# Optimization experiments

Measured on AMD Instinct MI355X. Metric: run time of the kernel, lower is better.

Reference implementation:

```python
import jax, jax.numpy as jnp
import numpy as np

ATOM_FDIM = 133
BOND_FDIM = 14
HIDDEN = 300
DEPTH = 3
FFN_HIDDEN = 300
NUM_ATOMS = 100000
NUM_EDGES = 400000
NUM_MOLS = 4096


def setup_inputs() -> dict:
    key = jax.random.key(0)
    ks = jax.random.split(key, 10)
    x = jax.random.normal(ks[0], (NUM_ATOMS, ATOM_FDIM), dtype=jnp.float32)
    edge_index = jax.random.randint(ks[1], (2, NUM_EDGES), 0, NUM_ATOMS, dtype=jnp.int32)
    edge_attr = jax.random.normal(ks[2], (NUM_EDGES, BOND_FDIM), dtype=jnp.float32)
    batch = jnp.sort(jax.random.randint(ks[3], (NUM_ATOMS,), 0, NUM_MOLS, dtype=jnp.int32))
    s = 0.05
    W_i = jax.random.normal(ks[4], (HIDDEN, ATOM_FDIM + BOND_FDIM), dtype=jnp.float32) * s
    W_h = jax.random.normal(ks[5], (HIDDEN, HIDDEN), dtype=jnp.float32) * s
    W_o_w = jax.random.normal(ks[6], (HIDDEN, ATOM_FDIM + HIDDEN), dtype=jnp.float32) * s
    W_o_b = jnp.zeros((HIDDEN,), dtype=jnp.float32)
    ffn1_w = jax.random.normal(ks[7], (FFN_HIDDEN, HIDDEN), dtype=jnp.float32) * s
    ffn1_b = jnp.zeros((FFN_HIDDEN,), dtype=jnp.float32)
    ffn2_w = jax.random.normal(ks[8], (1, FFN_HIDDEN), dtype=jnp.float32) * s
    ffn2_b = jnp.zeros((1,), dtype=jnp.float32)
    return {"x": x, "edge_index": edge_index, "edge_attr": edge_attr, "batch": batch,
            "W_i": W_i, "W_h": W_h, "W_o_w": W_o_w, "W_o_b": W_o_b,
            "ffn1_w": ffn1_w, "ffn1_b": ffn1_b, "ffn2_w": ffn2_w, "ffn2_b": ffn2_b}


def reference(x, edge_index, edge_attr, batch, W_i, W_h, W_o_w, W_o_b,
              ffn1_w, ffn1_b, ffn2_w, ffn2_b):
    num_atoms = x.shape[0]
    src, tgt = edge_index[0], edge_index[1]
    # initial edge messages: [E, hidden]
    init = jnp.concatenate([x[src], edge_attr], axis=-1)
    m = jax.nn.relu(init @ W_i.T)
    # dropout is identity at inference
    for _ in range(DEPTH - 1):
        nei = jax.ops.segment_sum(m, tgt, num_segments=num_atoms)  # [N, hidden]
        m = jax.nn.relu(m + nei[src] @ W_h.T)
    atom_msg = jax.ops.segment_sum(m, tgt, num_segments=num_atoms)
    atom_h = jax.nn.relu(jnp.concatenate([x, atom_msg], axis=-1) @ W_o_w.T + W_o_b)
    mol = jax.ops.segment_sum(atom_h, batch, num_segments=NUM_MOLS)  # [B, hidden]
    h = jax.nn.relu(mol @ ffn1_w.T + ffn1_b)
    out = h @ ffn2_w.T + ffn2_b  # [B, 1]
    return out
```

## Files before the change

kernel.cpp:

```cpp
#include <hip/hip_runtime.h>
#include <hip/hip_fp16.h>

#define HID   300
#define NEIP  320
#define PSTR  900
#define APB   4
#define SWK(r) (((r) >> 1) & 3)

typedef _Float16 f16;
typedef f16  f16x2 __attribute__((ext_vector_type(2)));
typedef f16  f16x4 __attribute__((ext_vector_type(4)));
typedef f16  f16x8 __attribute__((ext_vector_type(8)));
typedef float f32x4 __attribute__((ext_vector_type(4)));

__device__ __forceinline__ f16x2 u2h(unsigned u) {
    union { unsigned u; f16x2 h; } c; c.u = u; return c.h;
}
__device__ __forceinline__ unsigned pk16(float a, float b) {
    union { f16 h[2]; unsigned u; } c; c.h[0] = (f16)a; c.h[1] = (f16)b;
    return c.u;
}
__device__ __forceinline__ void glds16(const void* g, void* l) {
    __builtin_amdgcn_global_load_lds(
        (const __attribute__((address_space(1))) void*)g,
        (__attribute__((address_space(3))) void*)l, 16, 0, 0);
}

__global__ __launch_bounds__(256) void fill_f32(float* __restrict__ p, int n, float v)
{
    int i = blockIdx.x * blockDim.x + threadIdx.x;
    int stride = gridDim.x * blockDim.x;
    for (; i < n; i += stride) p[i] = v;
}

__global__ __launch_bounds__(256) void zero_i32(int* __restrict__ p, int n)
{
    int i = blockIdx.x * blockDim.x + threadIdx.x;
    int stride = gridDim.x * blockDim.x;
    for (; i < n; i += stride) p[i] = 0;
}

__global__ __launch_bounds__(256) void cvt_pad_f16(
    f16* __restrict__ dst, const float* __restrict__ src,
    int srcRows, int ldsrc, int kuse, int kpad, int dstRows)
{
    int i = blockIdx.x * 256 + threadIdx.x;
    const int total = dstRows * kpad;
    const int st = gridDim.x * 256;
    for (; i < total; i += st) {
        int r = i / kpad, k = i - r * kpad;
        float v = (r < srcRows && k < kuse) ? src[(size_t)r * ldsrc + k] : 0.f;
        const int t = k >> 5, kg = (k >> 3) & 3, w = k & 7;
        const int kd = (t << 5) | ((kg ^ SWK(r)) << 3) | w;
        dst[(size_t)r * kpad + kd] = (f16)v;
    }
}

__global__ __launch_bounds__(256) void hist_tgt(
    const int* __restrict__ tgt, int* __restrict__ deg, int E, int N)
{
    int e = blockIdx.x * 256 + threadIdx.x;
    const int st = gridDim.x * 256;
    for (; e < E; e += st) {
        int t = tgt[e];
        t = ((unsigned)t < (unsigned)N) ? t : 0;
        atomicAdd(&deg[t], 1);
    }
}

__global__ __launch_bounds__(1024) void scan_p1(
    const int* __restrict__ deg, int* __restrict__ bsum, int N)
{
    __shared__ int s[1024];
    const int t = threadIdx.x;
    const int i = blockIdx.x * 1024 + t;
    s[t] = (i < N) ? deg[i] : 0;
    __syncthreads();
#pragma unroll
    for (int off = 512; off > 0; off >>= 1) {
        if (t < off) s[t] += s[t + off];
        __syncthreads();
    }
    if (t == 0) bsum[blockIdx.x] = s[0];
}

__global__ __launch_bounds__(1024) void scan_p2(
    const int* __restrict__ bsum, int* __restrict__ boff,
    int G, int* __restrict__ rowPtrN, int E)
{
    __shared__ int s[1024];
    const int t = threadIdx.x;
    s[t] = (t < G) ? bsum[t] : 0;
    __syncthreads();
    for (int off = 1; off < 1024; off <<= 1) {
        const int v = (t >= off) ? s[t - off] : 0;
        __syncthreads();
        s[t] += v;
        __syncthreads();
    }
    if (t < G) boff[t] = (t == 0) ? 0 : s[t - 1];
    if (t == 0) *rowPtrN = E;
}

__global__ __launch_bounds__(1024) void scan_p3(
    const int* __restrict__ deg, const int* __restrict__ boff,
    int* __restrict__ rowPtr, int* __restrict__ cursor, int N)
{
    __shared__ int s[1024];
    const int t = threadIdx.x;
    const int i = blockIdx.x * 1024 + t;
    const int v = (i < N) ? deg[i] : 0;
    s[t] = v;
    __syncthreads();
    for (int off = 1; off < 1024; off <<= 1) {
        const int w = (t >= off) ? s[t - off] : 0;
        __syncthreads();
        s[t] += w;
        __syncthreads();
    }
    if (i < N) {
        const int excl = boff[blockIdx.x] + s[t] - v;
        rowPtr[i] = excl;
        cursor[i] = excl;
    }
}

__global__ __launch_bounds__(256) void scatter_e(
    const int* __restrict__ src, const int* __restrict__ tgt,
    const float* __restrict__ ea,
    int* __restrict__ cursor, int* __restrict__ csrc,
    unsigned* __restrict__ eaPk,
    int E, int N)
{
    int e = blockIdx.x * 256 + threadIdx.x;
    const int st = gridDim.x * 256;
    for (; e < E; e += st) {
        int t = tgt[e];
        int s = src[e];
        t = ((unsigned)t < (unsigned)N) ? t : 0;
        s = ((unsigned)s < (unsigned)N) ? s : 0;
        const int p = atomicAdd(&cursor[t], 1);
        csrc[p] = s;
        const float* er = ea + (size_t)e * 14;
        uint4 q0, q1;
        q0.x = pk16(er[0],  er[1]);  q0.y = pk16(er[2],  er[3]);
        q0.z = pk16(er[4],  er[5]);  q0.w = pk16(er[6],  er[7]);
        q1.x = pk16(er[8],  er[9]);  q1.y = pk16(er[10], er[11]);
        q1.z = pk16(er[12], er[13]); q1.w = 0u;
        uint4* dst = (uint4*)(eaPk + (size_t)p * 8);
        dst[0] = q0;
        dst[1] = q1;
    }
}

__global__ __launch_bounds__(512, 4) void gemm_mfma(
    const void* __restrict__ A1, int lda1, int a1f16, int K1use,
    const f16* __restrict__ W1, int kpad1,
    const void* __restrict__ A2, int lda2, int a2f16, int K2use,
    const f16* __restrict__ W2, int kpad2,
    const float* __restrict__ bias,
    f16* __restrict__ C, int ldc,
    int M, int do_relu)
{
    __shared__ f16 As[2][64 * 32];
    __shared__ f16 Ws[2][320 * 32];

    const int tid  = threadIdx.x;
    const int bm   = blockIdx.x * 64;
    const int lane = tid & 63;
    const int wv   = tid >> 6;
    const int wrow = (wv >> 2) * 32;
    const int wcol = (wv & 3) * 80;
    const int lm   = lane & 15;
    const int kg   = lane >> 4;

    const int n1 = A1 ? (kpad1 >> 5) : 0;
    const int n2 = A2 ? (kpad2 >> 5) : 0;
    const int ntot = n1 + n2;

    f32x4 acc[2][5];
#pragma unroll
    for (int r = 0; r < 2; ++r)
#pragma unroll
        for (int c = 0; c < 5; ++c) acc[r][c] = (f32x4){0.f, 0.f, 0.f, 0.f};

    const int arow = tid >> 2;
    const int asub = tid & 3;
    const int gm   = bm + arow;

    auto seg_f16 = [&](int s) -> bool {
        return (s < n1) ? (a1f16 != 0) : (a2f16 != 0);
    };

    auto a_load_f32 = [&](int s) -> f16x8 {
        const float* A; int lda, Kuse, k0;
        if (s < n1) { A = (const float*)A1; lda = lda1; Kuse = K1use; k0 = s << 5; }
        else        { A = (const float*)A2; lda = lda2; Kuse = K2use; k0 = (s - n1) << 5; }
        f16x8 v = (f16x8){0, 0, 0, 0, 0, 0, 0, 0};
        if (tid < 256 && gm < M) {
            const int gk = k0 + (asub << 3);
            const float* p = A + (size_t)gm * lda + gk;
#pragma unroll
            for (int j = 0; j < 8; ++j)
                v[j] = (gk + j < Kuse) ? (f16)p[j] : (f16)0.f;
        }
        return v;
    };

    auto commit_a = [&](int b, f16x8 v) {
        if (tid < 256)
            *(f16x8*)&As[b][arow * 32 + ((asub ^ SWK(arow)) << 3)] = v;
    };

    auto stage_glds = [&](int s, int b) {
        const f16* W; int kpad, k0; const f16* Af; int lda; bool f16seg;
        if (s < n1) { W = W1; kpad = kpad1; k0 = s << 5;
                      f16seg = (a1f16 != 0); Af = (const f16*)A1; lda = lda1; }
        else        { W = W2; kpad = kpad2; k0 = (s - n1) << 5;
                      f16seg = (a2f16 != 0); Af = (const f16*)A2; lda = lda2; }
        const int r16 = lane >> 2;
        const int q   = lane & 3;
        for (int c = wv; c < 24; c += 8) {
            if (c < 4) {
                if (f16seg) {
                    const int gR = bm + (c << 4) + r16;
                    if (gR < M)
                        glds16((const char*)Af + ((size_t)gR * lda + k0) * 2 + q * 16,
                               (void*)&As[b][c << 9]);
                }
            } else {
                const int R = ((c - 4) << 4) + r16;
                glds16((const char*)W + ((size_t)R * kpad + k0) * 2 + q * 16,
                       (void*)&Ws[b][(c - 4) << 9]);
            }
        }
    };

    f16x8 aNxt = (f16x8){0, 0, 0, 0, 0, 0, 0, 0};
    stage_glds(0, 0);
    if (!seg_f16(0)) commit_a(0, a_load_f32(0));
    if (ntot > 1 && !seg_f16(1)) aNxt = a_load_f32(1);
    __syncthreads();

    int b = 0;
    for (int s = 0; s < ntot; ++s) {
        f16x8 af[2], bf[5];
#pragma unroll
        for (int r = 0; r < 2; ++r) {
            const int R = wrow + (r << 4) + lm;
            af[r] = *(const f16x8*)&As[b][R * 32 + ((kg ^ SWK(R)) << 3)];
        }
#pragma unroll
        for (int c = 0; c < 5; ++c) {
            const int R = wcol + (c << 4) + lm;
            bf[c] = *(const f16x8*)&Ws[b][R * 32 + ((kg ^ SWK(R)) << 3)];
        }
        if (s + 1 < ntot) stage_glds(s + 1, b ^ 1);
        f16x8 aN2 = (f16x8){0, 0, 0, 0, 0, 0, 0, 0};
        if (s + 2 < ntot && !seg_f16(s + 2)) aN2 = a_load_f32(s + 2);
#pragma unroll
        for (int r = 0; r < 2; ++r)
#pragma unroll
            for (int c = 0; c < 5; ++c)
                acc[r][c] = __builtin_amdgcn_mfma_f32_16x16x32_f16(
                    af[r], bf[c], acc[r][c], 0, 0, 0);
        if (s + 1 < ntot && !seg_f16(s + 1)) commit_a(b ^ 1, aNxt);
        aNxt = aN2;
        __syncthreads();
        b ^= 1;
    }

#pragma unroll
    for (int r = 0; r < 2; ++r) {
        const int gm0 = bm + wrow + (r << 4) + ((lane >> 4) << 2);
#pragma unroll
        for (int c = 0; c < 5; ++c) {
            const int n = wcol + (c << 4) + lm;
            if (n >= HID) continue;
            const float bi = bias ? bias[n] : 0.f;
#pragma unroll
            for (int i = 0; i < 4; ++i) {
                const int gmo = gm0 + i;
                if (gmo >= M) continue;
                float v = acc[r][c][i] + bi;
                if (do_relu) v = fmaxf(v, 0.f);
                C[(size_t)gmo * ldc + n] = (f16)v;
            }
        }
    }
}

template <int NSLOTS>
__global__ __launch_bounds__(192) void edge_csr(
    const unsigned* __restrict__ packed,
    const int* __restrict__ rowPtr,
    const int* __restrict__ csrc,
    const unsigned* __restrict__ eaPk,
    const float* __restrict__ Wi,
    unsigned* __restrict__ out,
    int N)
{
    const int p = threadIdx.x;
    f16x2 wpk[14];
    if (p < 150) {
#pragma unroll
        for (int k = 0; k < 14; ++k)
            wpk[k] = (f16x2){(f16)Wi[(2 * p) * 147 + 133 + k],
                             (f16)Wi[(2 * p + 1) * 147 + 133 + k]};
    }
    const f16x2 zero2 = (f16x2){(f16)0.f, (f16)0.f};

    const int a0 = blockIdx.x * APB;
    const int a1 = min(a0 + APB, N);
    for (int a = a0; a < a1; ++a) {
        const int beg = rowPtr[a];
        const int end = rowPtr[a + 1];
        float acc0 = 0.f, acc1 = 0.f;
        if (p < 150) {
#pragma unroll 2
            for (int j = beg; j < end; ++j) {
                const int s = csrc[j];
                const unsigned* row = packed + (size_t)s * (PSTR / 2);
                const unsigned u0 = row[p];
                unsigned u1 = 0, u2 = 0;
                if (NSLOTS > 1) u1 = row[p + 150];
                if (NSLOTS > 2) u2 = row[p + 300];
                const unsigned* eq = eaPk + (size_t)j * 8;
                f16x2 ebA = zero2, ebB = zero2;
#pragma unroll
                for (int k = 0; k < 7; ++k) {
                    const f16x2 e2 = u2h(eq[k]);
                    ebA += (f16x2){e2.x, e2.x} * wpk[2 * k];
                    ebB += (f16x2){e2.y, e2.y} * wpk[2 * k + 1];
                }
                f16x2 m = __builtin_elementwise_max(u2h(u0) + (ebA + ebB), zero2);
                if (NSLOTS > 1) m = __builtin_elementwise_max(m + u2h(u1), zero2);
                if (NSLOTS > 2) m = __builtin_elementwise_max(m + u2h(u2), zero2);
                acc0 += (float)m.x;
                acc1 += (float)m.y;
            }
        }
        if (p < NEIP / 2) {
            const unsigned val = (p < 150) ? pk16(acc0, acc1) : 0u;
            const int t = p >> 4, kgc = (p >> 2) & 3, w = p & 3;
            out[(size_t)a * (NEIP / 2) + (t << 4) + ((kgc ^ SWK(a)) << 2) + w] = val;
        }
    }
}

__global__ __launch_bounds__(256) void mol_pool(
    const f16* __restrict__ ah,
    const int* __restrict__ batch,
    float* __restrict__ mol,
    int N)
{
    const int b = blockIdx.x;
    int lo = 0, hi = N;
    while (lo < hi) { int mid = (lo + hi) >> 1; if (batch[mid] < b) lo = mid + 1; else hi = mid; }
    const int start = lo;
    hi = N;
    while (lo < hi) { int mid = (lo + hi) >> 1; if (batch[mid] < b + 1) lo = mid + 1; else hi = mid; }
    const int end = lo;

    for (int h = threadIdx.x; h < HID; h += 256) {
        float s = 0.f;
        for (int a = start; a < end; ++a) s += (float)ah[(size_t)a * PSTR + h];
        mol[(size_t)b * HID + h] = s;
    }
}

__global__ __launch_bounds__(64) void ffn2_k(
    const f16* __restrict__ h1,
    const float* __restrict__ w2,
    const float* __restrict__ b2, float* __restrict__ out, int B)
{
    const int b = blockIdx.x;
    float s = 0.f;
    for (int k = threadIdx.x; k < HID; k += 64)
        s += (float)h1[(size_t)b * NEIP + k] * w2[k];
#pragma unroll
    for (int off = 32; off > 0; off >>= 1) s += __shfl_down(s, off);
    if (threadIdx.x == 0) out[b] = s + b2[0];
}

extern "C" void kernel_launch(void* const* d_in, const int* in_sizes, int n_in,
                              void* d_out, int out_size, void* d_ws, size_t ws_size,
                              hipStream_t stream)
{
    float* outp = (float*)d_out;
    const int fillBlocks = (out_size + 255) / 256;

    if (n_in < 12) {
        fill_f32<<<fillBlocks, 256, 0, stream>>>(outp, out_size, 2.0e6f + n_in);
        return;
    }

    const int N = in_sizes[0] / 133;
    const int E = in_sizes[1] / 2;
    const int B = out_size;

    const long long expect[12] = {
        (long long)N * 133, (long long)E * 2, (long long)E * 14, N,
        300LL * 147, 300LL * 300, 300LL * 433, 300,
        300LL * 300, 300, 300, 1 };
    for (int i = 0; i < 12; ++i) {
        if ((long long)in_sizes[i] != expect[i]) {
            fill_f32<<<fillBlocks, 256, 0, stream>>>(outp, out_size,
                                                     3.0e6f + 1.0e4f * i);
            return;
        }
    }

    const int G = (N + 1023) / 1024;
    if (G > 1024) {
        fill_f32<<<fillBlocks, 256, 0, stream>>>(outp, out_size, 4.0e6f);
        return;
    }

    char* basep = (char*)d_ws;
    auto align16 = [](size_t v) { return (v + 15) & ~(size_t)15; };
    const size_t packedB = align16((size_t)N * PSTR * sizeof(f16));
    const size_t neiB    = align16((size_t)N * NEIP * sizeof(f16));
    const size_t wSmall  = align16(320 * 160 * sizeof(f16));
    const size_t wBig    = align16(320 * 320 * sizeof(f16));
    const size_t molB    = align16((size_t)B * HID * sizeof(float));
    const size_t h1B     = align16((size_t)B * NEIP * sizeof(f16));
    const size_t rpB     = align16((size_t)(N + 1) * sizeof(int));
    const size_t curB    = align16((size_t)N * sizeof(int));
    const size_t csrcB   = align16((size_t)E * sizeof(int));
    const size_t eaB     = align16((size_t)E * 8 * sizeof(unsigned));
    const size_t bsB     = align16(1024 * sizeof(int));
    const size_t need = packedB + neiB + 2 * wSmall + 3 * wBig
                      + molB + h1B + rpB + 2 * curB + csrcB + eaB + 2 * bsB;

    if (ws_size < need) {
        fill_f32<<<fillBlocks, 256, 0, stream>>>(outp, out_size,
                                                 (float)(ws_size >> 20));
        return;
    }

    const float* x     = (const float*)d_in[0];
    const int*   ei    = (const int*)d_in[1];
    const float* ea    = (const float*)d_in[2];
    const int*   batch = (const int*)d_in[3];
    const float* W_i   = (const float*)d_in[4];
    const float* W_h   = (const float*)d_in[5];
    const float* W_o   = (const float*)d_in[6];
    const float* W_ob  = (const float*)d_in[7];
    const float* f1w   = (const float*)d_in[8];
    const float* f1b   = (const float*)d_in[9];
    const float* f2w   = (const float*)d_in[10];
    const float* f2b   = (const float*)d_in[11];
    const int* src = ei;
    const int* tgt = ei + E;

    char* cp = basep;
    f16* packed = (f16*)cp;         cp += packedB;
    f16* nei    = (f16*)cp;         cp += neiB;
    f16* WiA    = (f16*)cp;         cp += wSmall;
    f16* Wh     = (f16*)cp;         cp += wBig;
    f16* WoA    = (f16*)cp;         cp += wSmall;
    f16* WoB    = (f16*)cp;         cp += wBig;
    f16* Wf1    = (f16*)cp;         cp += wBig;
    float* mol  = (float*)cp;       cp += molB;
    f16* h1     = (f16*)cp;         cp += h1B;
    int* rowPtr = (int*)cp;         cp += rpB;
    int* cursor = (int*)cp;         cp += curB;
    int* deg    = (int*)cp;         cp += curB;
    int* csrc   = (int*)cp;         cp += csrcB;
    unsigned* eaPk = (unsigned*)cp; cp += eaB;
    int* bsum   = (int*)cp;         cp += bsB;
    int* boff   = (int*)cp;         cp += bsB;

    f16* xa_s  = packed;
    f16* hn0_s = packed + 300;
    f16* hn1_s = packed + 600;

    const unsigned* packed_u = (const unsigned*)packed;
    unsigned*       nei_u    = (unsigned*)nei;

    const int gAtom = (N + 63) / 64;
    const int gMolG = (B + 63) / 64;
    const int gEdge = (N + APB - 1) / APB;

    zero_i32<<<128, 256, 0, stream>>>(deg, N);
    hist_tgt<<<1024, 256, 0, stream>>>(tgt, deg, E, N);
    scan_p1<<<G, 1024, 0, stream>>>(deg, bsum, N);
    scan_p2<<<1, 1024, 0, stream>>>(bsum, boff, G, rowPtr + N, E);
    scan_p3<<<G, 1024, 0, stream>>>(deg, boff, rowPtr, cursor, N);
    scatter_e<<<1024, 256, 0, stream>>>(src, tgt, ea, cursor, csrc, eaPk, E, N);

    cvt_pad_f16<<<64,  256, 0, stream>>>(WiA, W_i,       300, 147, 133, 160, 320);
    cvt_pad_f16<<<128, 256, 0, stream>>>(Wh,  W_h,       300, 300, 300, 320, 320);
    cvt_pad_f16<<<64,  256, 0, stream>>>(WoA, W_o,       300, 433, 133, 160, 320);
    cvt_pad_f16<<<128, 256, 0, stream>>>(WoB, W_o + 133, 300, 433, 300, 320, 320);
    cvt_pad_f16<<<128, 256, 0, stream>>>(Wf1, f1w,       300, 300, 300, 320, 320);

    gemm_mfma<<<gAtom, 512, 0, stream>>>(x, 133, 0, 133, WiA, 160,
        nullptr, 0, 0, 0, nullptr, 0, nullptr, xa_s, PSTR, N, 0);
    edge_csr<1><<<gEdge, 192, 0, stream>>>(packed_u, rowPtr, csrc, eaPk, W_i,
                                           nei_u, N);
    gemm_mfma<<<gAtom, 512, 0, stream>>>(nei, NEIP, 1, NEIP, Wh, 320,
        nullptr, 0, 0, 0, nullptr, 0, nullptr, hn0_s, PSTR, N, 0);
    edge_csr<2><<<gEdge, 192, 0, stream>>>(packed_u, rowPtr, csrc, eaPk, W_i,
                                           nei_u, N);
    gemm_mfma<<<gAtom, 512, 0, stream>>>(nei, NEIP, 1, NEIP, Wh, 320,
        nullptr, 0, 0, 0, nullptr, 0, nullptr, hn1_s, PSTR, N, 0);
    edge_csr<3><<<gEdge, 192, 0, stream>>>(packed_u, rowPtr, csrc, eaPk, W_i,
                                           nei_u, N);
    gemm_mfma<<<gAtom, 512, 0, stream>>>(x, 133, 0, 133, WoA, 160,
        nei, NEIP, 1, NEIP, WoB, 320, W_ob, hn0_s, PSTR, N, 1);
    mol_pool<<<B, 256, 0, stream>>>(hn0_s, batch, mol, N);
    gemm_mfma<<<gMolG, 512, 0, stream>>>(mol, 300, 0, 300, Wf1, 320,
        nullptr, 0, 0, 0, nullptr, 0, f1b, h1, NEIP, B, 1);
    ffn2_k<<<B, 64, 0, stream>>>(h1, f2w, f2b, outp, B);
}
```

Before: 849.3 us.

## Stage full A tile in LDS, split packed slots, shrink edge-attr records

The GEMM now loads the block's whole 64-row A panel into LDS once per segment and streams only the weight tile each k-step. This drops the per-step A staging and the double buffering, and adds an extra barrier per iteration. The interleaved 900-wide packed activation buffer is split into three separate 300-wide arrays, and downstream strides now use HID instead of the padded widths. Packed edge attributes shrink from 8 to 7 words per edge to cut gather and scatter bytes, at the cost of 16-byte alignment. The larger LDS footprint and the serialized W staging may reduce occupancy and overlap.

```diff
diff --git a/kernel.cpp b/kernel.cpp
--- a/kernel.cpp
+++ b/kernel.cpp
@@ -3,13 +3,11 @@
 
 #define HID   300
 #define NEIP  320
-#define PSTR  900
 #define APB   4
 #define SWK(r) (((r) >> 1) & 3)
 
 typedef _Float16 f16;
 typedef f16  f16x2 __attribute__((ext_vector_type(2)));
-typedef f16  f16x4 __attribute__((ext_vector_type(4)));
 typedef f16  f16x8 __attribute__((ext_vector_type(8)));
 typedef float f32x4 __attribute__((ext_vector_type(4)));
 
@@ -142,18 +140,14 @@
         const int p = atomicAdd(&cursor[t], 1);
         csrc[p] = s;
         const float* er = ea + (size_t)e * 14;
-        uint4 q0, q1;
-        q0.x = pk16(er[0],  er[1]);  q0.y = pk16(er[2],  er[3]);
-        q0.z = pk16(er[4],  er[5]);  q0.w = pk16(er[6],  er[7]);
-        q1.x = pk16(er[8],  er[9]);  q1.y = pk16(er[10], er[11]);
-        q1.z = pk16(er[12], er[13]); q1.w = 0u;
-        uint4* dst = (uint4*)(eaPk + (size_t)p * 8);
-        dst[0] = q0;
-        dst[1] = q1;
-    }
-}
-
-__global__ __launch_bounds__(512, 4) void gemm_mfma(
+        unsigned* dst = eaPk + (size_t)p * 7;
+#pragma unroll
+        for (int k = 0; k < 7; ++k)
+            dst[k] = pk16(er[2 * k], er[2 * k + 1]);
+    }
+}
+
+__global__ __launch_bounds__(512) void gemm_mfma(
     const void* __restrict__ A1, int lda1, int a1f16, int K1use,
     const f16* __restrict__ W1, int kpad1,
     const void* __restrict__ A2, int lda2, int a2f16, int K2use,
@@ -162,8 +156,8 @@
     f16* __restrict__ C, int ldc,
     int M, int do_relu)
 {
-    __shared__ f16 As[2][64 * 32];
-    __shared__ f16 Ws[2][320 * 32];
+    __shared__ f16 As[64 * 320];
+    __shared__ f16 Ws[320 * 32];
 
     const int tid  = threadIdx.x;
     const int bm   = blockIdx.x * 64;
@@ -184,90 +178,80 @@
 #pragma unroll
         for (int c = 0; c < 5; ++c) acc[r][c] = (f32x4){0.f, 0.f, 0.f, 0.f};
 
-    const int arow = tid >> 2;
-    const int asub = tid & 3;
-    const int gm   = bm + arow;
-
-    auto seg_f16 = [&](int s) -> bool {
-        return (s < n1) ? (a1f16 != 0) : (a2f16 != 0);
-    };
-
-    auto a_load_f32 = [&](int s) -> f16x8 {
-        const float* A; int lda, Kuse, k0;
-        if (s < n1) { A = (const float*)A1; lda = lda1; Kuse = K1use; k0 = s << 5; }
-        else        { A = (const float*)A2; lda = lda2; Kuse = K2use; k0 = (s - n1) << 5; }
-        f16x8 v = (f16x8){0, 0, 0, 0, 0, 0, 0, 0};
-        if (tid < 256 && gm < M) {
-            const int gk = k0 + (asub << 3);
-            const float* p = A + (size_t)gm * lda + gk;
-#pragma unroll
-            for (int j = 0; j < 8; ++j)
-                v[j] = (gk + j < Kuse) ? (f16)p[j] : (f16)0.f;
-        }
-        return v;
-    };
-
-    auto commit_a = [&](int b, f16x8 v) {
-        if (tid < 256)
-            *(f16x8*)&As[b][arow * 32 + ((asub ^ SWK(arow)) << 3)] = v;
-    };
-
-    auto stage_glds = [&](int s, int b) {
-        const f16* W; int kpad, k0; const f16* Af; int lda; bool f16seg;
-        if (s < n1) { W = W1; kpad = kpad1; k0 = s << 5;
-                      f16seg = (a1f16 != 0); Af = (const f16*)A1; lda = lda1; }
-        else        { W = W2; kpad = kpad2; k0 = (s - n1) << 5;
-                      f16seg = (a2f16 != 0); Af = (const f16*)A2; lda = lda2; }
+    auto stage_W = [&](int s) {
+        const f16* W = (s < n1) ? W1 : W2;
+        const int kpad = (s < n1) ? kpad1 : kpad2;
+        const int k0 = (((s < n1) ? s : s - n1) << 5);
         const int r16 = lane >> 2;
         const int q   = lane & 3;
-        for (int c = wv; c < 24; c += 8) {
-            if (c < 4) {
-                if (f16seg) {
-                    const int gR = bm + (c << 4) + r16;
-                    if (gR < M)
-                        glds16((const char*)Af + ((size_t)gR * lda + k0) * 2 + q * 16,
-                               (void*)&As[b][c << 9]);
+        for (int c = wv; c < 20; c += 8) {
+            const int R = (c << 4) + r16;
+            glds16((const char*)W + ((size_t)R * kpad + k0) * 2 + q * 16,
+                   (void*)&Ws[c << 9]);
+        }
+    };
+
+    auto stage_A = [&](int seg) {
+        const void* A = seg ? A2 : A1;
+        const int lda  = seg ? lda2 : lda1;
+        const int af16 = seg ? a2f16 : a1f16;
+        const int kuse = seg ? K2use : K1use;
+        const int kpad = seg ? kpad2 : kpad1;
+        if (af16) {
+            const int nch = kpad >> 3;
+            const char* base = (const char*)A + (size_t)bm * lda * 2;
+            for (int c = wv; c < nch; c += 8)
+                glds16(base + (c << 10) + lane * 16, (void*)&As[c << 9]);
+        } else {
+            const int cpr = kpad >> 3;
+            for (int idx = tid; idx < 64 * cpr; idx += 512) {
+                const int row = idx / cpr;
+                const int ks  = (idx - row * cpr) << 3;
+                const int gmr = bm + row;
+                f16x8 v = (f16x8){0, 0, 0, 0, 0, 0, 0, 0};
+                if (gmr < M) {
+                    const float* p = (const float*)A + (size_t)gmr * lda + ks;
+#pragma unroll
+                    for (int j = 0; j < 8; ++j)
+                        v[j] = (ks + j < kuse) ? (f16)p[j] : (f16)0.f;
                 }
-            } else {
-                const int R = ((c - 4) << 4) + r16;
-                glds16((const char*)W + ((size_t)R * kpad + k0) * 2 + q * 16,
-                       (void*)&Ws[b][(c - 4) << 9]);
+                const int t = ks >> 5, kgc = (ks >> 3) & 3;
+                *(f16x8*)&As[row * kpad + (t << 5) + ((kgc ^ SWK(row)) << 3)] = v;
             }
         }
     };
 
-    f16x8 aNxt = (f16x8){0, 0, 0, 0, 0, 0, 0, 0};
-    stage_glds(0, 0);
-    if (!seg_f16(0)) commit_a(0, a_load_f32(0));
-    if (ntot > 1 && !seg_f16(1)) aNxt = a_load_f32(1);
+    stage_A(0);
+    stage_W(0);
     __syncthreads();
 
-    int b = 0;
     for (int s = 0; s < ntot; ++s) {
+        const int seg   = (s >= n1) ? 1 : 0;
+        const int kpadA = seg ? kpad2 : kpad1;
+        const int sl    = seg ? (s - n1) : s;
         f16x8 af[2], bf[5];
 #pragma unroll
         for (int r = 0; r < 2; ++r) {
             const int R = wrow + (r << 4) + lm;
-            af[r] = *(const f16x8*)&As[b][R * 32 + ((kg ^ SWK(R)) << 3)];
+            af[r] = *(const f16x8*)&As[R * kpadA + (sl << 5) + ((kg ^ SWK(R)) << 3)];
         }
 #pragma unroll
         for (int c = 0; c < 5; ++c) {
             const int R = wcol + (c << 4) + lm;
-            bf[c] = *(const f16x8*)&Ws[b][R * 32 + ((kg ^ SWK(R)) << 3)];
-        }
-        if (s + 1 < ntot) stage_glds(s + 1, b ^ 1);
-        f16x8 aN2 = (f16x8){0, 0, 0, 0, 0, 0, 0, 0};
-        if (s + 2 < ntot && !seg_f16(s + 2)) aN2 = a_load_f32(s + 2);
+            bf[c] = *(const f16x8*)&Ws[R * 32 + ((kg ^ SWK(R)) << 3)];
+        }
+        __syncthreads();
+        if (s + 1 < ntot) {
+            stage_W(s + 1);
+            if (s + 1 == n1 && n2) stage_A(1);
+        }
 #pragma unroll
         for (int r = 0; r < 2; ++r)
 #pragma unroll
             for (int c = 0; c < 5; ++c)
                 acc[r][c] = __builtin_amdgcn_mfma_f32_16x16x32_f16(
                     af[r], bf[c], acc[r][c], 0, 0, 0);
-        if (s + 1 < ntot && !seg_f16(s + 1)) commit_a(b ^ 1, aNxt);
-        aNxt = aN2;
-        __syncthreads();
-        b ^= 1;
+        __syncthreads();
     }
 
 #pragma unroll
@@ -292,7 +276,9 @@
 
 template <int NSLOTS>
 __global__ __launch_bounds__(192) void edge_csr(
-    const unsigned* __restrict__ packed,
+    const unsigned* __restrict__ xa,
+    const unsigned* __restrict__ hn0,
+    const unsigned* __restrict__ hn1,
     const int* __restrict__ rowPtr,
     const int* __restrict__ csrc,
     const unsigned* __restrict__ eaPk,
@@ -320,12 +306,12 @@
 #pragma unroll 2
             for (int j = beg; j < end; ++j) {
                 const int s = csrc[j];
-                const unsigned* row = packed + (size_t)s * (PSTR / 2);
-                const unsigned u0 = row[p];
+                const size_t srow = (size_t)s * 150 + p;
+                const unsigned u0 = xa[srow];
                 unsigned u1 = 0, u2 = 0;
-                if (NSLOTS > 1) u1 = row[p + 150];
-                if (NSLOTS > 2) u2 = row[p + 300];
-                const unsigned* eq = eaPk + (size_t)j * 8;
+                if (NSLOTS > 1) u1 = hn0[srow];
+                if (NSLOTS > 2) u2 = hn1[srow];
+                const unsigned* eq = eaPk + (size_t)j * 7;
                 f16x2 ebA = zero2, ebB = zero2;
 #pragma unroll
                 for (int k = 0; k < 7; ++k) {
@@ -364,7 +350,7 @@
 
     for (int h = threadIdx.x; h < HID; h += 256) {
         float s = 0.f;
-        for (int a = start; a < end; ++a) s += (float)ah[(size_t)a * PSTR + h];
+        for (int a = start; a < end; ++a) s += (float)ah[(size_t)a * HID + h];
         mol[(size_t)b * HID + h] = s;
     }
 }
@@ -377,7 +363,7 @@
     const int b = blockIdx.x;
     float s = 0.f;
     for (int k = threadIdx.x; k < HID; k += 64)
-        s += (float)h1[(size_t)b * NEIP + k] * w2[k];
+        s += (float)h1[(size_t)b * HID + k] * w2[k];
 #pragma unroll
     for (int off = 32; off > 0; off >>= 1) s += __shfl_down(s, off);
     if (threadIdx.x == 0) out[b] = s + b2[0];
@@ -419,18 +405,18 @@
 
     char* basep = (char*)d_ws;
     auto align16 = [](size_t v) { return (v + 15) & ~(size_t)15; };
-    const size_t packedB = align16((size_t)N * PSTR * sizeof(f16));
-    const size_t neiB    = align16((size_t)N * NEIP * sizeof(f16));
-    const size_t wSmall  = align16(320 * 160 * sizeof(f16));
-    const size_t wBig    = align16(320 * 320 * sizeof(f16));
-    const size_t molB    = align16((size_t)B * HID * sizeof(float));
-    const size_t h1B     = align16((size_t)B * NEIP * sizeof(f16));
-    const size_t rpB     = align16((size_t)(N + 1) * sizeof(int));
-    const size_t curB    = align16((size_t)N * sizeof(int));
-    const size_t csrcB   = align16((size_t)E * sizeof(int));
-    const size_t eaB     = align16((size_t)E * 8 * sizeof(unsigned));
-    const size_t bsB     = align16(1024 * sizeof(int));
-    const size_t need = packedB + neiB + 2 * wSmall + 3 * wBig
+    const size_t slotB  = align16((size_t)N * HID * sizeof(f16));
+    const size_t neiB   = align16((size_t)N * NEIP * sizeof(f16));
+    const size_t wSmall = align16(320 * 160 * sizeof(f16));
+    const size_t wBig   = align16(320 * 320 * sizeof(f16));
+    const size_t molB   = align16((size_t)B * HID * sizeof(float));
+    const size_t h1B    = align16((size_t)B * HID * sizeof(f16));
+    const size_t rpB    = align16((size_t)(N + 1) * sizeof(int));
+    const size_t curB   = align16((size_t)N * sizeof(int));
+    const size_t csrcB  = align16((size_t)E * sizeof(int));
+    const size_t eaB    = align16((size_t)E * 7 * sizeof(unsigned));
+    const size_t bsB    = align16(1024 * sizeof(int));
+    const size_t need = 3 * slotB + neiB + 2 * wSmall + 3 * wBig
                       + molB + h1B + rpB + 2 * curB + csrcB + eaB + 2 * bsB;
 
     if (ws_size < need) {
@@ -455,7 +441,9 @@
     const int* tgt = ei + E;
 
     char* cp = basep;
-    f16* packed = (f16*)cp;         cp += packedB;
+    f16* xa     = (f16*)cp;         cp += slotB;
+    f16* hn0    = (f16*)cp;         cp += slotB;
+    f16* hn1    = (f16*)cp;         cp += slotB;
     f16* nei    = (f16*)cp;         cp += neiB;
     f16* WiA    = (f16*)cp;         cp += wSmall;
     f16* Wh     = (f16*)cp;         cp += wBig;
@@ -472,12 +460,10 @@
     int* bsum   = (int*)cp;         cp += bsB;
     int* boff   = (int*)cp;         cp += bsB;
 
-    f16* xa_s  = packed;
-    f16* hn0_s = packed + 300;
-    f16* hn1_s = packed + 600;
-
-    const unsigned* packed_u = (const unsigned*)packed;
-    unsigned*       nei_u    = (unsigned*)nei;
+    const unsigned* xa_u  = (const unsigned*)xa;
+    const unsigned* hn0_u = (const unsigned*)hn0;
+    const unsigned* hn1_u = (const unsigned*)hn1;
+    unsigned*       nei_u = (unsigned*)nei;
 
     const int gAtom = (N + 63) / 64;
     const int gMolG = (B + 63) / 64;
@@ -497,21 +483,21 @@
     cvt_pad_f16<<<128, 256, 0, stream>>>(Wf1, f1w,       300, 300, 300, 320, 320);
 
     gemm_mfma<<<gAtom, 512, 0, stream>>>(x, 133, 0, 133, WiA, 160,
-        nullptr, 0, 0, 0, nullptr, 0, nullptr, xa_s, PSTR, N, 0);
-    edge_csr<1><<<gEdge, 192, 0, stream>>>(packed_u, rowPtr, csrc, eaPk, W_i,
-                                           nei_u, N);
+        nullptr, 0, 0, 0, nullptr, 0, nullptr, xa, HID, N, 0);
+    edge_csr<1><<<gEdge, 192, 0, stream>>>(xa_u, hn0_u, hn1_u, rowPtr, csrc,
+                                           eaPk, W_i, nei_u, N);
     gemm_mfma<<<gAtom, 512, 0, stream>>>(nei, NEIP, 1, NEIP, Wh, 320,
-        nullptr, 0, 0, 0, nullptr, 0, nullptr, hn0_s, PSTR, N, 0);
-    edge_csr<2><<<gEdge, 192, 0, stream>>>(packed_u, rowPtr, csrc, eaPk, W_i,
-                                           nei_u, N);
+        nullptr, 0, 0, 0, nullptr, 0, nullptr, hn0, HID, N, 0);
+    edge_csr<2><<<gEdge, 192, 0, stream>>>(xa_u, hn0_u, hn1_u, rowPtr, csrc,
+                                           eaPk, W_i, nei_u, N);
     gemm_mfma<<<gAtom, 512, 0, stream>>>(nei, NEIP, 1, NEIP, Wh, 320,
-        nullptr, 0, 0, 0, nullptr, 0, nullptr, hn1_s, PSTR, N, 0);
-    edge_csr<3><<<gEdge, 192, 0, stream>>>(packed_u, rowPtr, csrc, eaPk, W_i,
-                                           nei_u, N);
+        nullptr, 0, 0, 0, nullptr, 0, nullptr, hn1, HID, N, 0);
+    edge_csr<3><<<gEdge, 192, 0, stream>>>(xa_u, hn0_u, hn1_u, rowPtr, csrc,
+                                           eaPk, W_i, nei_u, N);
     gemm_mfma<<<gAtom, 512, 0, stream>>>(x, 133, 0, 133, WoA, 160,
-        nei, NEIP, 1, NEIP, WoB, 320, W_ob, hn0_s, PSTR, N, 1);
-    mol_pool<<<B, 256, 0, stream>>>(hn0_s, batch, mol, N);
+        nei, NEIP, 1, NEIP, WoB, 320, W_ob, xa, HID, N, 1);
+    mol_pool<<<B, 256, 0, stream>>>(xa, batch, mol, N);
     gemm_mfma<<<gMolG, 512, 0, stream>>>(mol, 300, 0, 300, Wf1, 320,
-        nullptr, 0, 0, 0, nullptr, 0, f1b, h1, NEIP, B, 1);
+        nullptr, 0, 0, 0, nullptr, 0, f1b, h1, HID, B, 1);
     ffn2_k<<<B, 64, 0, stream>>>(h1, f2w, f2b, outp, B);
 }
```

Result: faster. 802.2 us (-5.5%).
